# Performance work log

Measured on AMD Instinct MI355X. Metric: run time of the kernel, lower is better.

The kernel has to match this reference:

```python
import jax, jax.numpy as jnp
import numpy as np

B, NQ, NM = 8, 1024, 2048
DIM, HEADS, DHEAD, MLP = 512, 8, 64, 2048
INNER = HEADS * DHEAD
EPS = 1e-5


def layernorm(x, g, b):
    mu = jnp.mean(x, axis=-1, keepdims=True)
    var = jnp.mean(jnp.square(x - mu), axis=-1, keepdims=True)
    return (x - mu) * jax.lax.rsqrt(var + EPS) * g + b


def mha(q_in, k_in, v_in, wq, wk, wv, wo, bo, g, b):
    Bq, Nq, _ = q_in.shape
    Nk = k_in.shape[1]
    q = (q_in @ wq).reshape(Bq, Nq, HEADS, DHEAD)
    k = (k_in @ wk).reshape(Bq, Nk, HEADS, DHEAD)
    v = (v_in @ wv).reshape(Bq, Nk, HEADS, DHEAD)
    scale = DHEAD ** -0.5
    dots = jnp.einsum('bqhd,bkhd->bhqk', q, k) * scale
    attn = jax.nn.softmax(dots, axis=-1)
    out = jnp.einsum('bhqk,bkhd->bqhd', attn, v).reshape(Bq, Nq, INNER)
    out = out @ wo + bo
    return layernorm(out, g, b) + q_in


def ffn(x, w1, b1, w2, b2, g, b):
    h = jax.nn.relu(x @ w1 + b1)
    return layernorm(h @ w2 + b2, g, b) + x


def _mha_params(key, s=0.02):
    ks = jax.random.split(key, 4)
    return dict(
        wq=jax.random.normal(ks[0], (DIM, INNER), jnp.float32) * s,
        wk=jax.random.normal(ks[1], (DIM, INNER), jnp.float32) * s,
        wv=jax.random.normal(ks[2], (DIM, INNER), jnp.float32) * s,
        wo=jax.random.normal(ks[3], (INNER, DIM), jnp.float32) * s,
        bo=jnp.zeros((DIM,), jnp.float32),
        g=jnp.ones((DIM,), jnp.float32),
        b=jnp.zeros((DIM,), jnp.float32),
    )


def _ffn_params(key, s=0.02):
    ks = jax.random.split(key, 2)
    return dict(
        w1=jax.random.normal(ks[0], (DIM, MLP), jnp.float32) * s,
        b1=jnp.zeros((MLP,), jnp.float32),
        w2=jax.random.normal(ks[1], (MLP, DIM), jnp.float32) * s,
        b2=jnp.zeros((DIM,), jnp.float32),
        g=jnp.ones((DIM,), jnp.float32),
        b=jnp.zeros((DIM,), jnp.float32),
    )


def setup_inputs() -> dict:
    key = jax.random.key(0)
    ks = jax.random.split(key, 8)
    inp = {
        'tgt': jax.random.normal(ks[0], (B, NQ, DIM), jnp.float32),
        'memory': jax.random.normal(ks[1], (B, NM, DIM), jnp.float32),
        'pos': jax.random.normal(ks[2], (B, NM, DIM), jnp.float32),
        'query_pos': jax.random.normal(ks[3], (B, NQ, DIM), jnp.float32),
    }
    a0 = _mha_params(ks[4]); f0 = _ffn_params(ks[5])
    a1 = _mha_params(ks[6]); f1 = _ffn_params(ks[7])
    for name, d in (('a0', a0), ('f0', f0), ('a1', a1), ('f1', f1)):
        for k, v in d.items():
            inp[f'{name}_{k}'] = v
    return inp


def reference(tgt, memory, pos, query_pos,
              a0_wq, a0_wk, a0_wv, a0_wo, a0_bo, a0_g, a0_b,
              f0_w1, f0_b1, f0_w2, f0_b2, f0_g, f0_b,
              a1_wq, a1_wk, a1_wv, a1_wo, a1_bo, a1_g, a1_b,
              f1_w1, f1_b1, f1_w2, f1_b2, f1_g, f1_b):
    # self-attention: q=k=tgt+query_pos, v=tgt
    q0 = tgt + query_pos
    x = mha(q0, q0, tgt, a0_wq, a0_wk, a0_wv, a0_wo, a0_bo, a0_g, a0_b)
    x = ffn(x, f0_w1, f0_b1, f0_w2, f0_b2, f0_g, f0_b)
    # cross-attention: q=x+query_pos, k=memory+pos, v=memory
    q = x + query_pos
    k = memory + pos
    x = mha(q, k, memory, a1_wq, a1_wk, a1_wv, a1_wo, a1_bo, a1_g, a1_b)
    x = ffn(x, f1_w1, f1_b1, f1_w2, f1_b2, f1_g, f1_b)
    return x
```

## Files before the change

kernel.cpp:

```cpp
#include <hip/hip_runtime.h>
#include <stdint.h>
#include <stddef.h>

typedef __attribute__((ext_vector_type(8))) short short8;
typedef __attribute__((ext_vector_type(4))) short short4v;
typedef __attribute__((ext_vector_type(4))) float floatx4;

#define DEV __device__ __forceinline__

DEV float bf2f(short s) {
    union { float f; uint32_t u; } v;
    v.u = ((uint32_t)(uint16_t)s) << 16;
    return v.f;
}
DEV short f2bf(float f) {
    union { float f; uint32_t u; } v;
    v.f = f;
    uint32_t u = v.u + 0x7FFFu + ((v.u >> 16) & 1u);
    return (short)(u >> 16);
}
DEV short f2bf_tr(float f) {
    union { float f; uint32_t u; } v;
    v.f = f;
    return (short)(v.u >> 16);
}

template<int BIAS, int RELU, int OUTBF>
__global__ __launch_bounds__(256) void gemm_bt(
    const short* __restrict__ A, const short* __restrict__ Bt,
    const float* __restrict__ bias, void* __restrict__ Cout,
    int M, int N, int K)
{
    __shared__ short Alds[2][128 * 32];
    __shared__ short Blds[2][128 * 32];
    const int tid  = threadIdx.x;
    const int wave = tid >> 6, lane = tid & 63;
    const int g = lane >> 4, li = lane & 15;

    const int gx = gridDim.x;
    int flat = blockIdx.y * gx + blockIdx.x;
    const int nwg = gx * gridDim.y;
    flat = (flat & 7) * (nwg >> 3) + (flat >> 3);
    const long bm = (long)(flat % gx) * 128;
    const long bn = (long)(flat / gx) * 128;

    const int wr = (wave >> 1) * 64;
    const int wc = (wave & 1) * 64;
    const int srow = wave * 32 + (lane >> 2);
    const int scol = (lane & 3) * 8;
    const short* Ap = A + (bm + srow) * (long)K + scol;
    const short* Bp = Bt + (bn + srow) * (long)K + scol;

    auto STAGE = [&](int buf, int k0) {
        __builtin_amdgcn_global_load_lds(
            (const __attribute__((address_space(1))) void*)(Ap + k0),
            (__attribute__((address_space(3))) void*)(&Alds[buf][wave * 1024]), 16, 0, 0);
        __builtin_amdgcn_global_load_lds(
            (const __attribute__((address_space(1))) void*)(Ap + (long)16 * K + k0),
            (__attribute__((address_space(3))) void*)(&Alds[buf][wave * 1024 + 512]), 16, 0, 0);
        __builtin_amdgcn_global_load_lds(
            (const __attribute__((address_space(1))) void*)(Bp + k0),
            (__attribute__((address_space(3))) void*)(&Blds[buf][wave * 1024]), 16, 0, 0);
        __builtin_amdgcn_global_load_lds(
            (const __attribute__((address_space(1))) void*)(Bp + (long)16 * K + k0),
            (__attribute__((address_space(3))) void*)(&Blds[buf][wave * 1024 + 512]), 16, 0, 0);
    };

    floatx4 acc[4][4];
#pragma unroll
    for (int i = 0; i < 4; i++)
#pragma unroll
        for (int j = 0; j < 4; j++) acc[i][j] = (floatx4){0.f, 0.f, 0.f, 0.f};

    STAGE(0, 0);
    __syncthreads();
    int cur = 0;
    for (int k0 = 0; k0 < K; k0 += 32) {
        if (k0 + 32 < K) STAGE(cur ^ 1, k0 + 32);

        short8 af[4], bfr[4];
#pragma unroll
        for (int mi = 0; mi < 4; mi++)
            af[mi] = *(const short8*)(&Alds[cur][(wr + mi * 16 + li) * 32 + g * 8]);
#pragma unroll
        for (int ni = 0; ni < 4; ni++)
            bfr[ni] = *(const short8*)(&Blds[cur][(wc + ni * 16 + li) * 32 + g * 8]);
#pragma unroll
        for (int mi = 0; mi < 4; mi++)
#pragma unroll
            for (int ni = 0; ni < 4; ni++)
                acc[mi][ni] = __builtin_amdgcn_mfma_f32_16x16x32_bf16(
                    af[mi], bfr[ni], acc[mi][ni], 0, 0, 0);

        __syncthreads();
        cur ^= 1;
    }

    float* Cf = (float*)Cout;
    short* Cb = (short*)Cout;
#pragma unroll
    for (int mi = 0; mi < 4; mi++) {
#pragma unroll
        for (int ni = 0; ni < 4; ni++) {
            const long col = bn + wc + ni * 16 + li;
            const float bv = BIAS ? bias[col] : 0.f;
#pragma unroll
            for (int i = 0; i < 4; i++) {
                const long row = bm + wr + mi * 16 + g * 4 + i;
                float v = acc[mi][ni][i] + bv;
                if (RELU) v = fmaxf(v, 0.f);
                if (OUTBF) Cb[row * N + col] = f2bf(v);
                else       Cf[row * N + col] = v;
            }
        }
    }
}

__global__ __launch_bounds__(256) void gemm_bt2vt(
    const short* __restrict__ A0, const short* __restrict__ A1,
    const short* __restrict__ Bt, short* __restrict__ Cout,
    short* __restrict__ VT,
    int M, int N, int K, int nsplit, int ldc, int vtoff, int nkvlog)
{
    __shared__ short Alds[2][128 * 32];
    __shared__ short Blds[2][128 * 32];
    const int tid  = threadIdx.x;
    const int wave = tid >> 6, lane = tid & 63;
    const int g = lane >> 4, li = lane & 15;

    const int gx = gridDim.x;
    int flat = blockIdx.y * gx + blockIdx.x;
    const int nwg = gx * gridDim.y;
    flat = (flat & 7) * (nwg >> 3) + (flat >> 3);
    const long bm = (long)(flat % gx) * 128;
    const long bn = (long)(flat / gx) * 128;

    const int wr = (wave >> 1) * 64;
    const int wc = (wave & 1) * 64;
    const int srow = wave * 32 + (lane >> 2);
    const int scol = (lane & 3) * 8;
    const short* A = (bn < nsplit) ? A0 : A1;
    const short* Ap = A + (bm + srow) * (long)K + scol;
    const short* Bp = Bt + (bn + srow) * (long)K + scol;

    auto STAGE = [&](int buf, int k0) {
        __builtin_amdgcn_global_load_lds(
            (const __attribute__((address_space(1))) void*)(Ap + k0),
            (__attribute__((address_space(3))) void*)(&Alds[buf][wave * 1024]), 16, 0, 0);
        __builtin_amdgcn_global_load_lds(
            (const __attribute__((address_space(1))) void*)(Ap + (long)16 * K + k0),
            (__attribute__((address_space(3))) void*)(&Alds[buf][wave * 1024 + 512]), 16, 0, 0);
        __builtin_amdgcn_global_load_lds(
            (const __attribute__((address_space(1))) void*)(Bp + k0),
            (__attribute__((address_space(3))) void*)(&Blds[buf][wave * 1024]), 16, 0, 0);
        __builtin_amdgcn_global_load_lds(
            (const __attribute__((address_space(1))) void*)(Bp + (long)16 * K + k0),
            (__attribute__((address_space(3))) void*)(&Blds[buf][wave * 1024 + 512]), 16, 0, 0);
    };

    floatx4 acc[4][4];
#pragma unroll
    for (int i = 0; i < 4; i++)
#pragma unroll
        for (int j = 0; j < 4; j++) acc[i][j] = (floatx4){0.f, 0.f, 0.f, 0.f};

    STAGE(0, 0);
    __syncthreads();
    int cur = 0;
    for (int k0 = 0; k0 < K; k0 += 32) {
        if (k0 + 32 < K) STAGE(cur ^ 1, k0 + 32);
        short8 af[4], bfr[4];
#pragma unroll
        for (int mi = 0; mi < 4; mi++)
            af[mi] = *(const short8*)(&Alds[cur][(wr + mi * 16 + li) * 32 + g * 8]);
#pragma unroll
        for (int ni = 0; ni < 4; ni++)
            bfr[ni] = *(const short8*)(&Blds[cur][(wc + ni * 16 + li) * 32 + g * 8]);
#pragma unroll
        for (int mi = 0; mi < 4; mi++)
#pragma unroll
            for (int ni = 0; ni < 4; ni++)
                acc[mi][ni] = __builtin_amdgcn_mfma_f32_16x16x32_bf16(
                    af[mi], bfr[ni], acc[mi][ni], 0, 0, 0);
        __syncthreads();
        cur ^= 1;
    }

    if (bn < vtoff) {
#pragma unroll
        for (int mi = 0; mi < 4; mi++)
#pragma unroll
            for (int ni = 0; ni < 4; ni++) {
                const long col = bn + wc + ni * 16 + li;
#pragma unroll
                for (int i = 0; i < 4; i++) {
                    const long row = bm + wr + mi * 16 + g * 4 + i;
                    Cout[row * ldc + col] = f2bf(acc[mi][ni][i]);
                }
            }
    } else {
        const int mask = (1 << nkvlog) - 1;
#pragma unroll
        for (int mi = 0; mi < 4; mi++) {
            const int row0 = (int)(bm + wr + mi * 16 + g * 4);
            const int bb = row0 >> nkvlog;
            const int key0 = row0 & mask;
#pragma unroll
            for (int ni = 0; ni < 4; ni++) {
                const int d = (int)(bn + wc + ni * 16 + li) - vtoff;
                short4v o = { f2bf(acc[mi][ni][0]), f2bf(acc[mi][ni][1]),
                              f2bf(acc[mi][ni][2]), f2bf(acc[mi][ni][3]) };
                *(short4v*)(VT + ((long)(bb * 512 + d) << nkvlog) + key0) = o;
            }
        }
    }
}

template<int BIAS>
__global__ __launch_bounds__(256) void gemm_bt_sk(
    const short* __restrict__ A, const short* __restrict__ Bt,
    const float* __restrict__ bias, float* __restrict__ Cout,
    int M, int N, int K)
{
    __shared__ short Alds[2][128 * 32];
    __shared__ short Blds[2][128 * 32];
    const int tid  = threadIdx.x;
    const int wave = tid >> 6, lane = tid & 63;
    const int g = lane >> 4, li = lane & 15;
    const int z = blockIdx.z;
    const int Kh = K >> 1;

    const int gx = gridDim.x;
    int flat = blockIdx.y * gx + blockIdx.x;
    const int nwg = gx * gridDim.y;
    flat = (flat & 7) * (nwg >> 3) + (flat >> 3);
    const long bm = (long)(flat % gx) * 128;
    const long bn = (long)(flat / gx) * 128;

    const int wr = (wave >> 1) * 64;
    const int wc = (wave & 1) * 64;
    const int srow = wave * 32 + (lane >> 2);
    const int scol = (lane & 3) * 8;
    const short* Ap = A + (bm + srow) * (long)K + scol + (long)z * Kh;
    const short* Bp = Bt + (bn + srow) * (long)K + scol + (long)z * Kh;
    float* C = Cout + (long)z * M * N;

    auto STAGE = [&](int buf, int k0) {
        __builtin_amdgcn_global_load_lds(
            (const __attribute__((address_space(1))) void*)(Ap + k0),
            (__attribute__((address_space(3))) void*)(&Alds[buf][wave * 1024]), 16, 0, 0);
        __builtin_amdgcn_global_load_lds(
            (const __attribute__((address_space(1))) void*)(Ap + (long)16 * K + k0),
            (__attribute__((address_space(3))) void*)(&Alds[buf][wave * 1024 + 512]), 16, 0, 0);
        __builtin_amdgcn_global_load_lds(
            (const __attribute__((address_space(1))) void*)(Bp + k0),
            (__attribute__((address_space(3))) void*)(&Blds[buf][wave * 1024]), 16, 0, 0);
        __builtin_amdgcn_global_load_lds(
            (const __attribute__((address_space(1))) void*)(Bp + (long)16 * K + k0),
            (__attribute__((address_space(3))) void*)(&Blds[buf][wave * 1024 + 512]), 16, 0, 0);
    };

    floatx4 acc[4][4];
#pragma unroll
    for (int i = 0; i < 4; i++)
#pragma unroll
        for (int j = 0; j < 4; j++) acc[i][j] = (floatx4){0.f, 0.f, 0.f, 0.f};

    STAGE(0, 0);
    __syncthreads();
    int cur = 0;
    for (int k0 = 0; k0 < Kh; k0 += 32) {
        if (k0 + 32 < Kh) STAGE(cur ^ 1, k0 + 32);
        short8 af[4], bfr[4];
#pragma unroll
        for (int mi = 0; mi < 4; mi++)
            af[mi] = *(const short8*)(&Alds[cur][(wr + mi * 16 + li) * 32 + g * 8]);
#pragma unroll
        for (int ni = 0; ni < 4; ni++)
            bfr[ni] = *(const short8*)(&Blds[cur][(wc + ni * 16 + li) * 32 + g * 8]);
#pragma unroll
        for (int mi = 0; mi < 4; mi++)
#pragma unroll
            for (int ni = 0; ni < 4; ni++)
                acc[mi][ni] = __builtin_amdgcn_mfma_f32_16x16x32_bf16(
                    af[mi], bfr[ni], acc[mi][ni], 0, 0, 0);
        __syncthreads();
        cur ^= 1;
    }

#pragma unroll
    for (int mi = 0; mi < 4; mi++)
#pragma unroll
        for (int ni = 0; ni < 4; ni++) {
            const long col = bn + wc + ni * 16 + li;
            const float bv = (BIAS && z == 0) ? bias[col] : 0.f;
#pragma unroll
            for (int i = 0; i < 4; i++) {
                const long row = bm + wr + mi * 16 + g * 4 + i;
                C[row * N + col] = acc[mi][ni][i] + bv;
            }
        }
}

__global__ __launch_bounds__(256) void attn_kernel(
    const short* __restrict__ Qg, const short* __restrict__ Kg,
    const short* __restrict__ VTg, short* __restrict__ Og,
    int NQ, int NK, int ldq, int ldk)
{
    constexpr int LD = 68, LDP = 36;
    __shared__ short Klds[32 * LD];
    __shared__ short Vlds[64 * LD];
    __shared__ short Plds[4][32 * LDP];

    const int tid = threadIdx.x;
    const int wave = tid >> 6, lane = tid & 63;
    const int g = lane >> 4, li = lane & 15;

    const int nqb = NQ >> 7;
    const int i   = blockIdx.x;
    const int xcd = i & 7;
    const int t   = i >> 3;
    const int c   = t % nqb;
    const int gh  = t / nqb;
    const int grp = xcd + 8 * gh;
    const int b   = grp >> 3, h = grp & 7;
    const int q0  = c * 128 + wave * 32;

    const short* qptrA = Qg + ((long)(b * NQ + q0 + li) * ldq + h * 64);
    const short* qptrB = qptrA + (long)16 * ldq;
    short8 qfA[2], qfB[2];
#pragma unroll
    for (int f = 0; f < 2; f++) {
        short8 ta = *(const short8*)(qptrA + f * 32 + g * 8);
        short8 tb = *(const short8*)(qptrB + f * 32 + g * 8);
#pragma unroll
        for (int ii = 0; ii < 8; ii++) {
            ta[ii] = f2bf(bf2f(ta[ii]) * 0.18033688011112042f);
            tb[ii] = f2bf(bf2f(tb[ii]) * 0.18033688011112042f);
        }
        qfA[f] = ta; qfB[f] = tb;
    }

    floatx4 accA[4], accB[4];
#pragma unroll
    for (int s = 0; s < 4; s++) {
        accA[s] = (floatx4){0.f, 0.f, 0.f, 0.f};
        accB[s] = (floatx4){0.f, 0.f, 0.f, 0.f};
    }
    float lsumA = 0.f, lsumB = 0.f;

    const int skey = tid >> 3, sdc = (tid & 7) * 8;
    const int svd = tid >> 2, svk = (tid & 3) * 8;
    const short* kp = Kg + (long)b * NK * ldk + h * 64 + (long)skey * ldk + sdc;
    const short* vp = VTg + ((long)(b * 512 + h * 64 + svd)) * NK + svk;

    short8 kreg = *(const short8*)kp;  kp += (long)32 * ldk;
    short8 vreg = *(const short8*)vp;  vp += 32;

    for (int kt = 0; kt < NK; kt += 32) {
        __syncthreads();
        *(short8*)(Klds + skey * LD + sdc) = kreg;
        *(short8*)(Vlds + svd * LD + svk) = vreg;
        __syncthreads();
        if (kt + 32 < NK) {
            kreg = *(const short8*)kp;  kp += (long)32 * ldk;
            vreg = *(const short8*)vp;  vp += 32;
        }

        floatx4 sA0 = (floatx4){0.f, 0.f, 0.f, 0.f};
        floatx4 sA1 = (floatx4){0.f, 0.f, 0.f, 0.f};
        floatx4 sB0 = (floatx4){0.f, 0.f, 0.f, 0.f};
        floatx4 sB1 = (floatx4){0.f, 0.f, 0.f, 0.f};
        {
            short8 k00 = *(const short8*)(Klds + li * LD + g * 8);
            short8 k01 = *(const short8*)(Klds + li * LD + 32 + g * 8);
            short8 k10 = *(const short8*)(Klds + (16 + li) * LD + g * 8);
            short8 k11 = *(const short8*)(Klds + (16 + li) * LD + 32 + g * 8);
            __builtin_amdgcn_s_setprio(1);
            sA0 = __builtin_amdgcn_mfma_f32_16x16x32_bf16(k00, qfA[0], sA0, 0, 0, 0);
            sA0 = __builtin_amdgcn_mfma_f32_16x16x32_bf16(k01, qfA[1], sA0, 0, 0, 0);
            sA1 = __builtin_amdgcn_mfma_f32_16x16x32_bf16(k10, qfA[0], sA1, 0, 0, 0);
            sA1 = __builtin_amdgcn_mfma_f32_16x16x32_bf16(k11, qfA[1], sA1, 0, 0, 0);
            sB0 = __builtin_amdgcn_mfma_f32_16x16x32_bf16(k00, qfB[0], sB0, 0, 0, 0);
            sB0 = __builtin_amdgcn_mfma_f32_16x16x32_bf16(k01, qfB[1], sB0, 0, 0, 0);
            sB1 = __builtin_amdgcn_mfma_f32_16x16x32_bf16(k10, qfB[0], sB1, 0, 0, 0);
            sB1 = __builtin_amdgcn_mfma_f32_16x16x32_bf16(k11, qfB[1], sB1, 0, 0, 0);
            __builtin_amdgcn_s_setprio(0);
        }

        const float a0 = exp2f(sA0[0]), a1 = exp2f(sA0[1]);
        const float a2 = exp2f(sA0[2]), a3 = exp2f(sA0[3]);
        const float a4 = exp2f(sA1[0]), a5 = exp2f(sA1[1]);
        const float a6 = exp2f(sA1[2]), a7 = exp2f(sA1[3]);
        lsumA += ((a0 + a1) + (a2 + a3)) + ((a4 + a5) + (a6 + a7));
        const float b0 = exp2f(sB0[0]), b1 = exp2f(sB0[1]);
        const float b2 = exp2f(sB0[2]), b3 = exp2f(sB0[3]);
        const float b4 = exp2f(sB1[0]), b5 = exp2f(sB1[1]);
        const float b6 = exp2f(sB1[2]), b7 = exp2f(sB1[3]);
        lsumB += ((b0 + b1) + (b2 + b3)) + ((b4 + b5) + (b6 + b7));

        short4v pa0 = { f2bf_tr(a0), f2bf_tr(a1), f2bf_tr(a2), f2bf_tr(a3) };
        short4v pa1 = { f2bf_tr(a4), f2bf_tr(a5), f2bf_tr(a6), f2bf_tr(a7) };
        short4v pb0 = { f2bf_tr(b0), f2bf_tr(b1), f2bf_tr(b2), f2bf_tr(b3) };
        short4v pb1 = { f2bf_tr(b4), f2bf_tr(b5), f2bf_tr(b6), f2bf_tr(b7) };
        *(short4v*)(Plds[wave] + li * LDP + g * 4) = pa0;
        *(short4v*)(Plds[wave] + li * LDP + 16 + g * 4) = pa1;
        *(short4v*)(Plds[wave] + (16 + li) * LDP + g * 4) = pb0;
        *(short4v*)(Plds[wave] + (16 + li) * LDP + 16 + g * 4) = pb1;
        short8 pfA = *(const short8*)(Plds[wave] + li * LDP + g * 8);
        short8 pfB = *(const short8*)(Plds[wave] + (16 + li) * LDP + g * 8);

        __builtin_amdgcn_s_setprio(1);
#pragma unroll
        for (int s = 0; s < 4; s++) {
            short8 vf = *(const short8*)(Vlds + (s * 16 + li) * LD + g * 8);
            accA[s] = __builtin_amdgcn_mfma_f32_16x16x32_bf16(vf, pfA, accA[s], 0, 0, 0);
            accB[s] = __builtin_amdgcn_mfma_f32_16x16x32_bf16(vf, pfB, accB[s], 0, 0, 0);
        }
        __builtin_amdgcn_s_setprio(0);
    }

    lsumA += __shfl_xor(lsumA, 16);
    lsumA += __shfl_xor(lsumA, 32);
    lsumB += __shfl_xor(lsumB, 16);
    lsumB += __shfl_xor(lsumB, 32);
    const float invA = 1.f / lsumA;
    const float invB = 1.f / lsumB;
    short* optrA = Og + ((long)(b * NQ + q0 + li) * 512 + h * 64);
    short* optrB = optrA + (long)16 * 512;
#pragma unroll
    for (int s = 0; s < 4; s++) {
        short4v oa = { f2bf(accA[s][0] * invA), f2bf(accA[s][1] * invA),
                       f2bf(accA[s][2] * invA), f2bf(accA[s][3] * invA) };
        short4v ob = { f2bf(accB[s][0] * invB), f2bf(accB[s][1] * invB),
                       f2bf(accB[s][2] * invB), f2bf(accB[s][3] * invB) };
        *(short4v*)(optrA + s * 16 + g * 4) = oa;
        *(short4v*)(optrB + s * 16 + g * 4) = ob;
    }
}

__global__ __launch_bounds__(256) void add_conv2(
    const float* __restrict__ a, const float* __restrict__ b,
    float* __restrict__ of, short* __restrict__ ob1, short* __restrict__ ob2)
{
    const long i = (long)(blockIdx.x * 256 + threadIdx.x) * 4;
    const float4 va = *(const float4*)(a + i);
    float4 vs = va;
    if (b) {
        const float4 vb = *(const float4*)(b + i);
        vs.x += vb.x; vs.y += vb.y; vs.z += vb.z; vs.w += vb.w;
    }
    if (of) *(float4*)(of + i) = vs;
    short4v o1 = { f2bf(vs.x), f2bf(vs.y), f2bf(vs.z), f2bf(vs.w) };
    *(short4v*)(ob1 + i) = o1;
    if (ob2) {
        short4v o2 = { f2bf(va.x), f2bf(va.y), f2bf(va.z), f2bf(va.w) };
        *(short4v*)(ob2 + i) = o2;
    }
}

__global__ __launch_bounds__(256) void ln_res_kernel(
    const float* __restrict__ X, const float* __restrict__ X2,
    const float* __restrict__ gam, const float* __restrict__ bet,
    const float* __restrict__ res, const float* __restrict__ postadd,
    float* __restrict__ outF, short* __restrict__ outB)
{
    const int row = blockIdx.x * 4 + (threadIdx.x >> 6);
    const int lane = threadIdx.x & 63;
    const long base = (long)row * 512 + lane * 8;
    float x[8];
    *(float4*)(x) = *(const float4*)(X + base);
    *(float4*)(x + 4) = *(const float4*)(X + base + 4);
    if (X2) {
        float x2[8];
        *(float4*)(x2) = *(const float4*)(X2 + base);
        *(float4*)(x2 + 4) = *(const float4*)(X2 + base + 4);
#pragma unroll
        for (int i = 0; i < 8; i++) x[i] += x2[i];
    }
    float s = x[0] + x[1] + x[2] + x[3] + x[4] + x[5] + x[6] + x[7];
#pragma unroll
    for (int o = 1; o < 64; o <<= 1) s += __shfl_xor(s, o);
    const float mu = s * (1.0f / 512.0f);
    float vs = 0.f;
#pragma unroll
    for (int i = 0; i < 8; i++) { const float d = x[i] - mu; vs += d * d; }
#pragma unroll
    for (int o = 1; o < 64; o <<= 1) vs += __shfl_xor(vs, o);
    const float rs = rsqrtf(vs * (1.0f / 512.0f) + 1e-5f);

    float gv[8], bv[8], rv[8];
    *(float4*)(gv) = *(const float4*)(gam + lane * 8);
    *(float4*)(gv + 4) = *(const float4*)(gam + lane * 8 + 4);
    *(float4*)(bv) = *(const float4*)(bet + lane * 8);
    *(float4*)(bv + 4) = *(const float4*)(bet + lane * 8 + 4);
    *(float4*)(rv) = *(const float4*)(res + base);
    *(float4*)(rv + 4) = *(const float4*)(res + base + 4);

    float y[8];
#pragma unroll
    for (int i = 0; i < 8; i++) y[i] = (x[i] - mu) * rs * gv[i] + bv[i] + rv[i];
    if (postadd) {
        float pv[8];
        *(float4*)(pv) = *(const float4*)(postadd + base);
        *(float4*)(pv + 4) = *(const float4*)(postadd + base + 4);
#pragma unroll
        for (int i = 0; i < 8; i++) y[i] += pv[i];
    }
    *(float4*)(outF + base) = *(float4*)(y);
    *(float4*)(outF + base + 4) = *(float4*)(y + 4);
    if (outB) {
        short8 ob;
#pragma unroll
        for (int i = 0; i < 8; i++) ob[i] = f2bf(y[i]);
        *(short8*)(outB + base) = ob;
    }
}

__global__ __launch_bounds__(256) void wtrans8(
    const float* __restrict__ w0, const float* __restrict__ w1,
    const float* __restrict__ w2, const float* __restrict__ w3,
    const float* __restrict__ w4, const float* __restrict__ w5,
    const float* __restrict__ w6, const float* __restrict__ w7,
    short* __restrict__ o0, short* __restrict__ o1,
    short* __restrict__ o2, short* __restrict__ o3,
    short* __restrict__ o4, short* __restrict__ o5,
    short* __restrict__ o6, short* __restrict__ o7,
    int K, int N)
{
    const float* Ws[8] = {w0, w1, w2, w3, w4, w5, w6, w7};
    short* Os[8] = {o0, o1, o2, o3, o4, o5, o6, o7};
    const float* W = Ws[blockIdx.z];
    short* Wt = Os[blockIdx.z];
    __shared__ short t[32][33];
    const int n0 = blockIdx.x * 32, k0 = blockIdx.y * 32;
    const int tx = threadIdx.x & 31, ty = threadIdx.x >> 5;
    for (int r = ty; r < 32; r += 8)
        t[r][tx] = f2bf(W[(long)(k0 + r) * N + n0 + tx]);
    __syncthreads();
    for (int r = ty; r < 32; r += 8)
        Wt[(long)(n0 + r) * K + k0 + tx] = t[tx][r];
}

extern "C" void kernel_launch(void* const* d_in, const int* in_sizes, int n_in,
                              void* d_out, int out_size, void* d_ws, size_t ws_size,
                              hipStream_t stream)
{
    (void)in_sizes; (void)n_in; (void)out_size; (void)ws_size;
    const float* tgt   = (const float*)d_in[0];
    const float* mem   = (const float*)d_in[1];
    const float* pos   = (const float*)d_in[2];
    const float* qpos  = (const float*)d_in[3];
    const float* a0_wq = (const float*)d_in[4];
    const float* a0_wk = (const float*)d_in[5];
    const float* a0_wv = (const float*)d_in[6];
    const float* a0_wo = (const float*)d_in[7];
    const float* a0_bo = (const float*)d_in[8];
    const float* a0_g  = (const float*)d_in[9];
    const float* a0_b  = (const float*)d_in[10];
    const float* f0_w1 = (const float*)d_in[11];
    const float* f0_b1 = (const float*)d_in[12];
    const float* f0_w2 = (const float*)d_in[13];
    const float* f0_b2 = (const float*)d_in[14];
    const float* f0_g  = (const float*)d_in[15];
    const float* f0_b  = (const float*)d_in[16];
    const float* a1_wq = (const float*)d_in[17];
    const float* a1_wk = (const float*)d_in[18];
    const float* a1_wv = (const float*)d_in[19];
    const float* a1_wo = (const float*)d_in[20];
    const float* a1_bo = (const float*)d_in[21];
    const float* a1_g  = (const float*)d_in[22];
    const float* a1_b  = (const float*)d_in[23];
    const float* f1_w1 = (const float*)d_in[24];
    const float* f1_b1 = (const float*)d_in[25];
    const float* f1_w2 = (const float*)d_in[26];
    const float* f1_b2 = (const float*)d_in[27];
    const float* f1_g  = (const float*)d_in[28];
    const float* f1_b  = (const float*)d_in[29];

    const int M1 = 8 * 1024;
    const int M2 = 8 * 2048;
    const size_t MB = 1ull << 20;
    char* ws = (char*)d_ws;

    float* resid = (float*)(ws + 0 * MB);
    float* xf    = (float*)(ws + 16 * MB);
    short* xb    = (short*)(ws + 32 * MB);
    short* wb    = (short*)(ws + 40 * MB);
    short* a0_wqt = wb;            short* a0_wkt = wb + 262144;
    short* a0_wvt = wb + 524288;   short* a0_wot = wb + 786432;
    short* f0_w1t = wb + 1048576;  short* f0_w2t = wb + 2097152;
    short* a1_wqt = wb + 3145728;  short* a1_wkt = wb + 3407872;
    short* a1_wvt = wb + 3670016;  short* a1_wot = wb + 3932160;
    short* f1_w1t = wb + 4194304;  short* f1_w2t = wb + 5242880;
    char* S = ws + 56 * MB;

    wtrans8<<<dim3(16, 16, 8), 256, 0, stream>>>(
        a0_wq, a0_wk, a0_wv, a0_wo, a1_wq, a1_wk, a1_wv, a1_wo,
        a0_wqt, a0_wkt, a0_wvt, a0_wot, a1_wqt, a1_wkt, a1_wvt, a1_wot, 512, 512);
    wtrans8<<<dim3(64, 16, 2), 256, 0, stream>>>(
        f0_w1, f1_w1, nullptr, nullptr, nullptr, nullptr, nullptr, nullptr,
        f0_w1t, f1_w1t, nullptr, nullptr, nullptr, nullptr, nullptr, nullptr, 512, 2048);
    wtrans8<<<dim3(16, 64, 2), 256, 0, stream>>>(
        f0_w2, f1_w2, nullptr, nullptr, nullptr, nullptr, nullptr, nullptr,
        f0_w2t, f1_w2t, nullptr, nullptr, nullptr, nullptr, nullptr, nullptr, 2048, 512);

    short* QKs  = (short*)(S + 0 * MB);
    short* VsT  = (short*)(S + 16 * MB);
    short* AOs  = (short*)(S + 24 * MB);
    float* P0a  = (float*)(S + 32 * MB);
    float* P1a  = (float*)(S + 48 * MB);
    short* q0b  = (short*)(S + 64 * MB);
    short* tgtb = (short*)(S + 72 * MB);

    add_conv2<<<4096, 256, 0, stream>>>(tgt, qpos, resid, q0b, tgtb);

    gemm_bt2vt<<<dim3(64, 12), 256, 0, stream>>>(q0b, tgtb, a0_wqt, QKs, VsT,
                                                 M1, 1536, 512, 1024, 1024, 1024, 10);
    attn_kernel<<<512, 256, 0, stream>>>(QKs, QKs + 512, VsT, AOs,
                                         1024, 1024, 1024, 1024);
    gemm_bt_sk<1><<<dim3(64, 4, 2), 256, 0, stream>>>(AOs, a0_wot, a0_bo, P0a,
                                                      M1, 512, 512);
    ln_res_kernel<<<2048, 256, 0, stream>>>(P0a, P1a, a0_g, a0_b, resid, nullptr, xf, xb);

    short* Hb  = (short*)(S + 0 * MB);
    float* P0f = (float*)(S + 32 * MB);
    float* P1f = (float*)(S + 48 * MB);
    short* qcb = (short*)(S + 80 * MB);
    gemm_bt<1,1,1><<<dim3(64, 16), 256, 0, stream>>>(xb, f0_w1t, f0_b1, Hb, M1, 2048, 512);
    gemm_bt_sk<1><<<dim3(64, 4, 2), 256, 0, stream>>>(Hb, f0_w2t, f0_b2, P0f,
                                                      M1, 512, 2048);
    ln_res_kernel<<<2048, 256, 0, stream>>>(P0f, P1f, f0_g, f0_b, xf, qpos, resid, qcb);

    short* kcb  = (short*)(S + 0 * MB);
    short* memb = (short*)(S + 16 * MB);
    short* Kc   = (short*)(S + 32 * MB);
    short* VcT  = (short*)(S + 48 * MB);
    short* Qc   = (short*)(S + 64 * MB);
    short* AOc  = (short*)(S + 72 * MB);
    float* P0c  = (float*)(S + 32 * MB);
    float* P1c  = (float*)(S + 48 * MB);

    add_conv2<<<8192, 256, 0, stream>>>(mem, pos, nullptr, kcb, memb);

    gemm_bt<0,0,1><<<dim3(64, 4), 256, 0, stream>>>(qcb, a1_wqt, nullptr, Qc, M1, 512, 512);
    gemm_bt2vt<<<dim3(128, 8), 256, 0, stream>>>(kcb, memb, a1_wkt, Kc, VcT,
                                                 M2, 1024, 512, 512, 512, 512, 11);
    attn_kernel<<<512, 256, 0, stream>>>(Qc, Kc, VcT, AOc,
                                         1024, 2048, 512, 512);
    gemm_bt_sk<1><<<dim3(64, 4, 2), 256, 0, stream>>>(AOc, a1_wot, a1_bo, P0c,
                                                      M1, 512, 512);
    ln_res_kernel<<<2048, 256, 0, stream>>>(P0c, P1c, a1_g, a1_b, resid, nullptr, xf, xb);

    short* Hb2  = (short*)(S + 0 * MB);
    float* P0g  = (float*)(S + 32 * MB);
    float* P1g  = (float*)(S + 48 * MB);
    gemm_bt<1,1,1><<<dim3(64, 16), 256, 0, stream>>>(xb, f1_w1t, f1_b1, Hb2, M1, 2048, 512);
    gemm_bt_sk<1><<<dim3(64, 4, 2), 256, 0, stream>>>(Hb2, f1_w2t, f1_b2, P0g,
                                                      M1, 512, 2048);
    ln_res_kernel<<<2048, 256, 0, stream>>>(P0g, P1g, f1_g, f1_b, xf, nullptr,
                                            (float*)d_out, nullptr);
}
```

Measured before the change: 432.1 us.

## Split attention over key halves with fp32 partials and a combine kernel

The attention kernel now takes a second grid dimension that splits the key/value sequence into two halves. Each half writes unnormalized fp32 output partials and per-row softmax denominators to scratch memory, reusing buffers whose earlier contents are already consumed. A new combine kernel adds the two halves, normalizes and converts to bf16 for the output projection. This doubles the number of attention blocks to fill the GPU better and halves each block's serial key loop, at the cost of roughly 32 MB of extra fp32 writes and reads plus an extra launch per attention layer.

```diff
diff --git a/kernel.cpp b/kernel.cpp
--- a/kernel.cpp
+++ b/kernel.cpp
@@ -304,7 +304,8 @@
 
 __global__ __launch_bounds__(256) void attn_kernel(
     const short* __restrict__ Qg, const short* __restrict__ Kg,
-    const short* __restrict__ VTg, short* __restrict__ Og,
+    const short* __restrict__ VTg, float* __restrict__ Opart,
+    float* __restrict__ Lpart,
     int NQ, int NK, int ldq, int ldk)
 {
     constexpr int LD = 68, LDP = 36;
@@ -315,6 +316,9 @@
     const int tid = threadIdx.x;
     const int wave = tid >> 6, lane = tid & 63;
     const int g = lane >> 4, li = lane & 15;
+    const int z = blockIdx.y;
+    const int NKh = NK >> 1;
+    const int Mtot = NQ * 8;
 
     const int nqb = NQ >> 7;
     const int i   = blockIdx.x;
@@ -351,18 +355,19 @@
 
     const int skey = tid >> 3, sdc = (tid & 7) * 8;
     const int svd = tid >> 2, svk = (tid & 3) * 8;
-    const short* kp = Kg + (long)b * NK * ldk + h * 64 + (long)skey * ldk + sdc;
-    const short* vp = VTg + ((long)(b * 512 + h * 64 + svd)) * NK + svk;
+    const short* kp = Kg + (long)b * NK * ldk + h * 64
+                      + (long)(z * NKh + skey) * ldk + sdc;
+    const short* vp = VTg + ((long)(b * 512 + h * 64 + svd)) * NK + z * NKh + svk;
 
     short8 kreg = *(const short8*)kp;  kp += (long)32 * ldk;
     short8 vreg = *(const short8*)vp;  vp += 32;
 
-    for (int kt = 0; kt < NK; kt += 32) {
+    for (int kt = 0; kt < NKh; kt += 32) {
         __syncthreads();
         *(short8*)(Klds + skey * LD + sdc) = kreg;
         *(short8*)(Vlds + svd * LD + svk) = vreg;
         __syncthreads();
-        if (kt + 32 < NK) {
+        if (kt + 32 < NKh) {
             kreg = *(const short8*)kp;  kp += (long)32 * ldk;
             vreg = *(const short8*)vp;  vp += 32;
         }
@@ -424,19 +429,41 @@
     lsumA += __shfl_xor(lsumA, 32);
     lsumB += __shfl_xor(lsumB, 16);
     lsumB += __shfl_xor(lsumB, 32);
-    const float invA = 1.f / lsumA;
-    const float invB = 1.f / lsumB;
-    short* optrA = Og + ((long)(b * NQ + q0 + li) * 512 + h * 64);
-    short* optrB = optrA + (long)16 * 512;
+
+    float* optrA = Opart + ((long)z * Mtot + b * NQ + q0 + li) * 512 + h * 64;
+    float* optrB = optrA + (long)16 * 512;
 #pragma unroll
     for (int s = 0; s < 4; s++) {
-        short4v oa = { f2bf(accA[s][0] * invA), f2bf(accA[s][1] * invA),
-                       f2bf(accA[s][2] * invA), f2bf(accA[s][3] * invA) };
-        short4v ob = { f2bf(accB[s][0] * invB), f2bf(accB[s][1] * invB),
-                       f2bf(accB[s][2] * invB), f2bf(accB[s][3] * invB) };
-        *(short4v*)(optrA + s * 16 + g * 4) = oa;
-        *(short4v*)(optrB + s * 16 + g * 4) = ob;
-    }
+        *(float4*)(optrA + s * 16 + g * 4) = *(float4*)&accA[s];
+        *(float4*)(optrB + s * 16 + g * 4) = *(float4*)&accB[s];
+    }
+    if (g == 0) {
+        Lpart[((long)z * Mtot + b * NQ + q0 + li) * 8 + h] = lsumA;
+        Lpart[((long)z * Mtot + b * NQ + q0 + 16 + li) * 8 + h] = lsumB;
+    }
+}
+
+__global__ __launch_bounds__(256) void attn_combine(
+    const float* __restrict__ Op, const float* __restrict__ Lp,
+    short* __restrict__ AO)
+{
+    const int row = blockIdx.x * 4 + (threadIdx.x >> 6);
+    const int lane = threadIdx.x & 63;
+    const long base = (long)row * 512 + lane * 8;
+    const int h = lane >> 3;
+    const long RZ = (long)8192 * 512;
+    const float l = Lp[row * 8 + h] + Lp[65536 + row * 8 + h];
+    const float inv = 1.f / l;
+    float4 a0 = *(const float4*)(Op + base);
+    float4 a1 = *(const float4*)(Op + base + 4);
+    float4 c0 = *(const float4*)(Op + RZ + base);
+    float4 c1 = *(const float4*)(Op + RZ + base + 4);
+    short8 o;
+    o[0] = f2bf((a0.x + c0.x) * inv); o[1] = f2bf((a0.y + c0.y) * inv);
+    o[2] = f2bf((a0.z + c0.z) * inv); o[3] = f2bf((a0.w + c0.w) * inv);
+    o[4] = f2bf((a1.x + c1.x) * inv); o[5] = f2bf((a1.y + c1.y) * inv);
+    o[6] = f2bf((a1.z + c1.z) * inv); o[7] = f2bf((a1.w + c1.w) * inv);
+    *(short8*)(AO + base) = o;
 }
 
 __global__ __launch_bounds__(256) void add_conv2(
@@ -610,15 +637,18 @@
     short* AOs  = (short*)(S + 24 * MB);
     float* P0a  = (float*)(S + 32 * MB);
     float* P1a  = (float*)(S + 48 * MB);
+    float* OpA  = (float*)(S + 32 * MB);
     short* q0b  = (short*)(S + 64 * MB);
+    float* LpA  = (float*)(S + 64 * MB);
     short* tgtb = (short*)(S + 72 * MB);
 
     add_conv2<<<4096, 256, 0, stream>>>(tgt, qpos, resid, q0b, tgtb);
 
     gemm_bt2vt<<<dim3(64, 12), 256, 0, stream>>>(q0b, tgtb, a0_wqt, QKs, VsT,
                                                  M1, 1536, 512, 1024, 1024, 1024, 10);
-    attn_kernel<<<512, 256, 0, stream>>>(QKs, QKs + 512, VsT, AOs,
-                                         1024, 1024, 1024, 1024);
+    attn_kernel<<<dim3(512, 2), 256, 0, stream>>>(QKs, QKs + 512, VsT, OpA, LpA,
+                                                  1024, 1024, 1024, 1024);
+    attn_combine<<<2048, 256, 0, stream>>>(OpA, LpA, AOs);
     gemm_bt_sk<1><<<dim3(64, 4, 2), 256, 0, stream>>>(AOs, a0_wot, a0_bo, P0a,
                                                       M1, 512, 512);
     ln_res_kernel<<<2048, 256, 0, stream>>>(P0a, P1a, a0_g, a0_b, resid, nullptr, xf, xb);
@@ -634,10 +664,12 @@
 
     short* kcb  = (short*)(S + 0 * MB);
     short* memb = (short*)(S + 16 * MB);
+    float* OpC  = (float*)(S + 0 * MB);
     short* Kc   = (short*)(S + 32 * MB);
     short* VcT  = (short*)(S + 48 * MB);
     short* Qc   = (short*)(S + 64 * MB);
     short* AOc  = (short*)(S + 72 * MB);
+    float* LpC  = (float*)(S + 80 * MB);
     float* P0c  = (float*)(S + 32 * MB);
     float* P1c  = (float*)(S + 48 * MB);
 
@@ -646,8 +678,9 @@
     gemm_bt<0,0,1><<<dim3(64, 4), 256, 0, stream>>>(qcb, a1_wqt, nullptr, Qc, M1, 512, 512);
     gemm_bt2vt<<<dim3(128, 8), 256, 0, stream>>>(kcb, memb, a1_wkt, Kc, VcT,
                                                  M2, 1024, 512, 512, 512, 512, 11);
-    attn_kernel<<<512, 256, 0, stream>>>(Qc, Kc, VcT, AOc,
-                                         1024, 2048, 512, 512);
+    attn_kernel<<<dim3(512, 2), 256, 0, stream>>>(Qc, Kc, VcT, OpC, LpC,
+                                                  1024, 2048, 512, 512);
+    attn_combine<<<2048, 256, 0, stream>>>(OpC, LpC, AOc);
     gemm_bt_sk<1><<<dim3(64, 4, 2), 256, 0, stream>>>(AOc, a1_wot, a1_bo, P0c,
                                                       M1, 512, 512);
     ln_res_kernel<<<2048, 256, 0, stream>>>(P0c, P1c, a1_g, a1_b, resid, nullptr, xf, xb);
```

After: 434.4 us. Within noise of the previous version (+0.5%).
